# Optimization experiments

Measured on AMD Instinct MI355X. Metric: run time of the kernel, lower is better.

## Reference

```python
import jax, jax.numpy as jnp
import numpy as np

N_NODES = 100000
N_EDGES = 3200000
IN_CH = 256
OUT_CH = 10


def setup_inputs() -> dict:
    key = jax.random.key(0)
    k1, k2, k3, k4 = jax.random.split(key, 4)
    x = jax.random.normal(k1, (N_NODES, IN_CH), dtype=jnp.float32)
    edge_index = jax.random.randint(k2, (2, N_EDGES), 0, N_NODES, dtype=jnp.int64)
    W_mu = jax.random.normal(k3, (IN_CH, OUT_CH), dtype=jnp.float32) * (1.0 / np.sqrt(IN_CH))
    b_mu = jnp.zeros((OUT_CH,), dtype=jnp.float32)
    W_logstd = jax.random.normal(k4, (IN_CH, OUT_CH), dtype=jnp.float32) * (1.0 / np.sqrt(IN_CH))
    b_logstd = jnp.zeros((OUT_CH,), dtype=jnp.float32)
    return {"x": x, "edge_index": edge_index, "W_mu": W_mu, "b_mu": b_mu,
            "W_logstd": W_logstd, "b_logstd": b_logstd}


def _gcn_norm(edge_index, num_nodes):
    # PyG gcn_norm: add self loops, deg from target (col), norm = d^-1/2[row]*d^-1/2[col]
    loop = jnp.arange(num_nodes, dtype=edge_index.dtype)
    row = jnp.concatenate([edge_index[0], loop])  # source nodes
    col = jnp.concatenate([edge_index[1], loop])  # target nodes
    deg = jax.ops.segment_sum(jnp.ones_like(col, dtype=jnp.float32), col,
                              num_segments=num_nodes)
    dinv = jax.lax.rsqrt(jnp.maximum(deg, 1.0))  # self loops guarantee deg>=1
    norm = dinv[row] * dinv[col]  # [E+N]
    return row, col, norm


def _gcn_conv(x, W, b, row, col, norm, num_nodes):
    h = x @ W                               # [N, out]  linear transform first
    msg = h[row] * norm[:, None]            # gather + scale, [E+N, out]
    out = jax.ops.segment_sum(msg, col, num_segments=num_nodes)  # scatter-add
    return out + b


def reference(x, edge_index, W_mu, b_mu, W_logstd, b_logstd):
    n = x.shape[0]
    row, col, norm = _gcn_norm(edge_index, n)
    mu = _gcn_conv(x, W_mu, b_mu, row, col, norm, n)
    logstd = _gcn_conv(x, W_logstd, b_logstd, row, col, norm, n)
    return mu, logstd
```

## Files before the change

kernel.cpp:

```cpp
#include <hip/hip_runtime.h>
#include <math.h>

#define N_NODES 100000
#define N_EDGES 3200000
#define IN_CH 256
#define NC 20
#define OC 10
#define NPB 128
#define NBUCK 782
#define CAP 4864

#define CHUNK3 8192
#define NCHUNK3 391

__global__ __launch_bounds__(256) void k_initptr(int* __restrict__ bptr) {
    int i = blockIdx.x * 256 + threadIdx.x;
    if (i < NBUCK) bptr[i] = i * CAP;
}

__global__ __launch_bounds__(1024) void k_bin3(const int* __restrict__ row,
                                               const int* __restrict__ col,
                                               int* __restrict__ bptr,
                                               int* __restrict__ bpairs) {
    __shared__ int   lh[NBUCK];
    __shared__ int   lscan[NBUCK];
    __shared__ int   gmino[NBUCK];
    __shared__ int   stage[CHUNK3];
    __shared__ unsigned short sbkt[CHUNK3];

    int t = threadIdx.x;
    int e0 = blockIdx.x * CHUNK3;
    int nE = N_EDGES - e0; if (nE > CHUNK3) nE = CHUNK3;
    int n4 = nE >> 2;
    const int4* c4 = (const int4*)(col + e0);
    const int4* r4 = (const int4*)(row + e0);

    for (int i = t; i < NBUCK; i += 1024) lh[i] = 0;
    __syncthreads();

    for (int j = t; j < n4; j += 1024) {
        int4 c = c4[j];
        atomicAdd(&lh[c.x >> 7], 1); atomicAdd(&lh[c.y >> 7], 1);
        atomicAdd(&lh[c.z >> 7], 1); atomicAdd(&lh[c.w >> 7], 1);
    }
    __syncthreads();

    int cnt = 0;
    if (t < NBUCK) { cnt = lh[t]; lscan[t] = cnt; }
    __syncthreads();
    for (int o = 1; o < NBUCK; o <<= 1) {
        int add = 0;
        if (t < NBUCK && t >= o) add = lscan[t - o];
        __syncthreads();
        if (t < NBUCK) lscan[t] += add;
        __syncthreads();
    }
    if (t < NBUCK) {
        int lofs = lscan[t] - cnt;
        int gbase = cnt ? atomicAdd(&bptr[t], cnt) : 0;
        gmino[t] = gbase - lofs;
        lh[t] = lofs;
    }
    __syncthreads();

    for (int j = t; j < n4; j += 1024) {
        int4 c = c4[j];
        int4 r = r4[j];
        int b0 = c.x >> 7, b1 = c.y >> 7, b2 = c.z >> 7, b3 = c.w >> 7;
        int s0 = atomicAdd(&lh[b0], 1);
        int s1 = atomicAdd(&lh[b1], 1);
        int s2 = atomicAdd(&lh[b2], 1);
        int s3 = atomicAdd(&lh[b3], 1);
        stage[s0] = (r.x << 7) | (c.x & 127); sbkt[s0] = (unsigned short)b0;
        stage[s1] = (r.y << 7) | (c.y & 127); sbkt[s1] = (unsigned short)b1;
        stage[s2] = (r.z << 7) | (c.z & 127); sbkt[s2] = (unsigned short)b2;
        stage[s3] = (r.w << 7) | (c.w & 127); sbkt[s3] = (unsigned short)b3;
    }
    __syncthreads();

    for (int j = t; j < nE; j += 1024) {
        int b = sbkt[j];
        int dst = gmino[b] + j;
        if (dst < (b + 1) * CAP) bpairs[dst] = stage[j];
    }
}

__global__ __launch_bounds__(256) void k_deg(const int* __restrict__ bptr,
                                             const int* __restrict__ bpairs,
                                             float* __restrict__ dinv) {
    __shared__ int lc[NPB];
    int b = blockIdx.x, t = threadIdx.x;
    if (t < NPB) lc[t] = 0;
    __syncthreads();
    int start = b * CAP;
    int n = bptr[b] - start; if (n > CAP) n = CAP;
    for (int p = t; p < n; p += 256)
        atomicAdd(&lc[bpairs[start + p] & 127], 1);
    __syncthreads();
    int node = b * NPB + t;
    if (t < NPB && node < N_NODES)
        dinv[node] = rsqrtf((float)(lc[t] + 1));
}

__device__ __forceinline__ unsigned bfpack(float a, float b) {
    unsigned ua = __float_as_uint(a), ub = __float_as_uint(b);
    ua = (ua + 0x7FFFu + ((ua >> 16) & 1u)) >> 16;
    ub = (ub + 0x7FFFu + ((ub >> 16) & 1u)) >> 16;
    return ua | (ub << 16);
}
__device__ __forceinline__ float bflo(unsigned p) { return __uint_as_float(p << 16); }
__device__ __forceinline__ float bfhi(unsigned p) { return __uint_as_float(p & 0xFFFF0000u); }

__global__ __launch_bounds__(256) void k_gemm3(const float* __restrict__ x,
                                               const float* __restrict__ Wmu,
                                               const float* __restrict__ Wls,
                                               const float* __restrict__ dinv,
                                               unsigned* __restrict__ hbf) {
    __shared__ float sW[NC * 272];
    int t = threadIdx.x;
    for (int idx = t; idx < IN_CH * OC; idx += 256) {
        int k = idx / OC, c = idx - k * OC;
        int kk = k >> 6, j = k & 63;
        sW[c * 272 + kk * 68 + j]          = Wmu[idx];
        sW[(c + OC) * 272 + kk * 68 + j]   = Wls[idx];
    }
    __syncthreads();

    int kk = t & 3;
    int slot = t >> 2;
    int n0 = blockIdx.x * 256 + slot;

    int nd[4];
#pragma unroll
    for (int u = 0; u < 4; u++) {
        int n = n0 + u * 64;
        nd[u] = (n < N_NODES) ? n : (N_NODES - 1);
    }

    float acc[4][NC];
#pragma unroll
    for (int u = 0; u < 4; u++)
#pragma unroll
        for (int c = 0; c < NC; c++) acc[u][c] = 0.0f;

    const float4* x4 = (const float4*)x;

#pragma unroll 4
    for (int j4 = 0; j4 < 16; j4++) {
        float4 xv0 = x4[(size_t)nd[0] * 64 + kk * 16 + j4];
        float4 xv1 = x4[(size_t)nd[1] * 64 + kk * 16 + j4];
        float4 xv2 = x4[(size_t)nd[2] * 64 + kk * 16 + j4];
        float4 xv3 = x4[(size_t)nd[3] * 64 + kk * 16 + j4];
#pragma unroll
        for (int c = 0; c < NC; c++) {
            float4 w = *(const float4*)&sW[c * 272 + kk * 68 + j4 * 4];
            acc[0][c] += xv0.x * w.x + xv0.y * w.y + xv0.z * w.z + xv0.w * w.w;
            acc[1][c] += xv1.x * w.x + xv1.y * w.y + xv1.z * w.z + xv1.w * w.w;
            acc[2][c] += xv2.x * w.x + xv2.y * w.y + xv2.z * w.z + xv2.w * w.w;
            acc[3][c] += xv3.x * w.x + xv3.y * w.y + xv3.z * w.z + xv3.w * w.w;
        }
    }

#pragma unroll
    for (int u = 0; u < 4; u++)
#pragma unroll
        for (int c = 0; c < NC; c++) {
            acc[u][c] += __shfl_xor(acc[u][c], 2);
            acc[u][c] += __shfl_xor(acc[u][c], 1);
        }

    if (kk == 0) {
#pragma unroll
        for (int u = 0; u < 4; u++) {
            int n = n0 + u * 64;
            if (n >= N_NODES) continue;
            float d = dinv[n];
            unsigned* hp = hbf + (size_t)n * 10;
            *(uint2*)(hp + 0) = make_uint2(bfpack(acc[u][0] * d,  acc[u][1] * d),
                                           bfpack(acc[u][2] * d,  acc[u][3] * d));
            *(uint2*)(hp + 2) = make_uint2(bfpack(acc[u][4] * d,  acc[u][5] * d),
                                           bfpack(acc[u][6] * d,  acc[u][7] * d));
            *(uint2*)(hp + 4) = make_uint2(bfpack(acc[u][8] * d,  acc[u][9] * d),
                                           bfpack(acc[u][10] * d, acc[u][11] * d));
            *(uint2*)(hp + 6) = make_uint2(bfpack(acc[u][12] * d, acc[u][13] * d),
                                           bfpack(acc[u][14] * d, acc[u][15] * d));
            *(uint2*)(hp + 8) = make_uint2(bfpack(acc[u][16] * d, acc[u][17] * d),
                                           bfpack(acc[u][18] * d, acc[u][19] * d));
        }
    }
}

__global__ __launch_bounds__(256) void k_agg4(const int* __restrict__ bptr,
                                              const int* __restrict__ bpairs,
                                              const unsigned* __restrict__ hbf,
                                              const float* __restrict__ bmu,
                                              const float* __restrict__ bls,
                                              float* __restrict__ out) {
    __shared__ int lcnt[NPB];
    __shared__ int lscan[NPB];
    __shared__ int sCnt[NPB];
    __shared__ int ssrc[CAP];
    int b = blockIdx.x, t = threadIdx.x;
    int start = b * CAP;
    int n = bptr[b] - start; if (n > CAP) n = CAP;

    if (t < NPB) lcnt[t] = 0;
    __syncthreads();
    for (int p = t; p < n; p += 256)
        atomicAdd(&lcnt[bpairs[start + p] & 127], 1);
    __syncthreads();

    int cnt = 0;
    if (t < NPB) { cnt = lcnt[t]; lscan[t] = cnt; sCnt[t] = cnt; }
    __syncthreads();
    for (int o = 1; o < NPB; o <<= 1) {
        int add = 0;
        if (t < NPB && t >= o) add = lscan[t - o];
        __syncthreads();
        if (t < NPB) lscan[t] += add;
        __syncthreads();
    }
    if (t < NPB) lcnt[t] = lscan[t] - cnt;
    __syncthreads();

    for (int p = t; p < n; p += 256) {
        int pk = bpairs[start + p];
        int q = atomicAdd(&lcnt[pk & 127], 1);
        ssrc[q] = ((unsigned)pk) >> 7;
    }
    __syncthreads();

    int nl = t >> 1, half = t & 1;
    int node = b * NPB + nl;
    int ccnt = sCnt[nl];
    int base = lscan[nl] - ccnt;
    int mid = ccnt >> 1;
    int j0 = half ? mid : 0;
    int j1 = half ? ccnt : mid;

    float a[NC];
#pragma unroll
    for (int c = 0; c < NC; c++) a[c] = 0.0f;

#define ADDROW(R)                                                        \
    {                                                                    \
        const unsigned* hp_ = hbf + (size_t)(R) * 10;                    \
        uint2 q0 = *(const uint2*)(hp_ + 0);                             \
        uint2 q1 = *(const uint2*)(hp_ + 2);                             \
        uint2 q2 = *(const uint2*)(hp_ + 4);                             \
        uint2 q3 = *(const uint2*)(hp_ + 6);                             \
        uint2 q4 = *(const uint2*)(hp_ + 8);                             \
        a[0]  += bflo(q0.x); a[1]  += bfhi(q0.x);                        \
        a[2]  += bflo(q0.y); a[3]  += bfhi(q0.y);                        \
        a[4]  += bflo(q1.x); a[5]  += bfhi(q1.x);                        \
        a[6]  += bflo(q1.y); a[7]  += bfhi(q1.y);                        \
        a[8]  += bflo(q2.x); a[9]  += bfhi(q2.x);                        \
        a[10] += bflo(q2.y); a[11] += bfhi(q2.y);                        \
        a[12] += bflo(q3.x); a[13] += bfhi(q3.x);                        \
        a[14] += bflo(q3.y); a[15] += bfhi(q3.y);                        \
        a[16] += bflo(q4.x); a[17] += bfhi(q4.x);                        \
        a[18] += bflo(q4.y); a[19] += bfhi(q4.y);                        \
    }

    int j = j0;
    for (; j + 1 < j1; j += 2) {
        int r0 = ssrc[base + j];
        int r1 = ssrc[base + j + 1];
        ADDROW(r0);
        ADDROW(r1);
    }
    if (j < j1) {
        int r0 = ssrc[base + j];
        ADDROW(r0);
    }
    if (half == 0 && node < N_NODES) ADDROW(node);
#undef ADDROW

#pragma unroll
    for (int c = 0; c < NC; c++) a[c] += __shfl_xor(a[c], 1);

    if (half == 0 && node < N_NODES) {
        float dn = rsqrtf((float)(ccnt + 1));
        float* om = out + (size_t)node * OC;
        float* ol = out + (size_t)N_NODES * OC + (size_t)node * OC;
#pragma unroll
        for (int c = 0; c < OC; c++) {
            om[c] = dn * a[c]      + bmu[c];
            ol[c] = dn * a[c + OC] + bls[c];
        }
    }
}

__global__ __launch_bounds__(256) void k_init_deg(float* __restrict__ deg) {
    int i = blockIdx.x * 256 + threadIdx.x;
    if (i < N_NODES) deg[i] = 1.0f;
}
__global__ __launch_bounds__(256) void k_count(const int* __restrict__ col, float* __restrict__ deg) {
    int e = blockIdx.x * 256 + threadIdx.x;
    if (e < N_EDGES) atomicAdd(&deg[col[e]], 1.0f);
}
__global__ __launch_bounds__(256) void k_dinvk(float* __restrict__ deg) {
    int i = blockIdx.x * 256 + threadIdx.x;
    if (i < N_NODES) deg[i] = rsqrtf(deg[i]);
}
__global__ __launch_bounds__(256) void k_gemm_f32(const float* __restrict__ x,
                                                  const float* __restrict__ Wmu,
                                                  const float* __restrict__ Wls,
                                                  float* __restrict__ h) {
    int node = blockIdx.x * 256 + threadIdx.x;
    if (node >= N_NODES) return;
    const float4* x4 = (const float4*)(x + (size_t)node * IN_CH);
    float acc[NC];
#pragma unroll
    for (int c = 0; c < NC; c++) acc[c] = 0.0f;
    for (int k4 = 0; k4 < IN_CH / 4; k4++) {
        float4 xv = x4[k4];
        float xk[4] = {xv.x, xv.y, xv.z, xv.w};
#pragma unroll
        for (int kk = 0; kk < 4; kk++) {
            const float* wm = Wmu + (k4 * 4 + kk) * OC;
            const float* wl = Wls + (k4 * 4 + kk) * OC;
#pragma unroll
            for (int c = 0; c < OC; c++) {
                acc[c]      += xk[kk] * wm[c];
                acc[c + OC] += xk[kk] * wl[c];
            }
        }
    }
    float* hp = h + (size_t)node * NC;
#pragma unroll
    for (int c = 0; c < NC; c++) hp[c] = acc[c];
}
__global__ __launch_bounds__(256) void k_scatter(const int* __restrict__ row, const int* __restrict__ col,
                                                 const float* __restrict__ dinv, const float* __restrict__ h,
                                                 float* __restrict__ out) {
    int e = blockIdx.x * 256 + threadIdx.x;
    if (e >= N_EDGES) return;
    int r = row[e], c = col[e];
    float s = dinv[r] * dinv[c];
    const float* hp = h + (size_t)r * NC;
    float* om = out + (size_t)c * OC;
    float* ol = om + (size_t)N_NODES * OC;
#pragma unroll
    for (int k = 0; k < OC; k++) atomicAdd(om + k, hp[k] * s);
#pragma unroll
    for (int k = 0; k < OC; k++) atomicAdd(ol + k, hp[OC + k] * s);
}
__global__ __launch_bounds__(256) void k_final(const float* __restrict__ h, const float* __restrict__ dinv,
                                               const float* __restrict__ bmu, const float* __restrict__ bls,
                                               float* __restrict__ out) {
    int i = blockIdx.x * 256 + threadIdx.x;
    if (i >= N_NODES * OC) return;
    int node = i / OC, c = i - node * OC;
    float d = dinv[node];
    float d2 = d * d;
    out[i]                += h[node * NC + c]      * d2 + bmu[c];
    out[N_NODES * OC + i] += h[node * NC + OC + c] * d2 + bls[c];
}

extern "C" void kernel_launch(void* const* d_in, const int* in_sizes, int n_in,
                              void* d_out, int out_size, void* d_ws, size_t ws_size,
                              hipStream_t stream) {
    const float* x   = (const float*)d_in[0];
    const int*   ei  = (const int*)d_in[1];
    const float* Wmu = (const float*)d_in[2];
    const float* bmu = (const float*)d_in[3];
    const float* Wls = (const float*)d_in[4];
    const float* bls = (const float*)d_in[5];
    float* out = (float*)d_out;

    const int* row = ei;
    const int* col = ei + N_EDGES;

    const size_t BPAIRS_OFF = (size_t)(9 << 19);
    const size_t REQ = BPAIRS_OFF + (size_t)NBUCK * CAP * 4;

    if (ws_size >= REQ) {
        char* w = (char*)d_ws;
        int*      bptr   = (int*)(w);
        float*    dinv   = (float*)(w + 8192);
        unsigned* hbf    = (unsigned*)(w + (512 << 10));
        int*      bpairs = (int*)(w + BPAIRS_OFF);

        k_initptr<<<(NBUCK + 255) / 256, 256, 0, stream>>>(bptr);
        k_bin3<<<NCHUNK3, 1024, 0, stream>>>(row, col, bptr, bpairs);
        k_deg<<<NBUCK, 256, 0, stream>>>(bptr, bpairs, dinv);
        k_gemm3<<<(N_NODES + 255) / 256, 256, 0, stream>>>(x, Wmu, Wls, dinv, hbf);
        k_agg4<<<NBUCK, 256, 0, stream>>>(bptr, bpairs, hbf, bmu, bls, out);
    } else {
        float* deg = (float*)d_ws;
        float* h   = (float*)((char*)d_ws + (1 << 20));
        hipMemsetAsync(d_out, 0, (size_t)out_size * sizeof(float), stream);
        k_init_deg<<<(N_NODES + 255) / 256, 256, 0, stream>>>(deg);
        k_count<<<(N_EDGES + 255) / 256, 256, 0, stream>>>(col, deg);
        k_dinvk<<<(N_NODES + 255) / 256, 256, 0, stream>>>(deg);
        k_gemm_f32<<<(N_NODES + 255) / 256, 256, 0, stream>>>(x, Wmu, Wls, h);
        k_scatter<<<(N_EDGES + 255) / 256, 256, 0, stream>>>(row, col, deg, h, out);
        k_final<<<(N_NODES * OC + 255) / 256, 256, 0, stream>>>(h, deg, bmu, bls, out);
    }
}
```

Before: 265.6 us.

## Stage x tiles through shared memory with one node per thread in GEMM

Rewrites the small dense transform so each block loads 256-node by 32-channel tiles of x into padded shared memory with coalesced float4 reads. Each thread then owns one node and accumulates all 20 outputs, reading W as a wave-uniform broadcast from shared memory, which removes the cross-lane shuffle reduction. This trades the old per-thread strided global loads for more barriers and shared-memory traffic.

```diff
diff --git a/kernel.cpp b/kernel.cpp
--- a/kernel.cpp
+++ b/kernel.cpp
@@ -111,82 +111,68 @@
 __device__ __forceinline__ float bflo(unsigned p) { return __uint_as_float(p << 16); }
 __device__ __forceinline__ float bfhi(unsigned p) { return __uint_as_float(p & 0xFFFF0000u); }
 
-__global__ __launch_bounds__(256) void k_gemm3(const float* __restrict__ x,
+__global__ __launch_bounds__(256) void k_gemm5(const float* __restrict__ x,
                                                const float* __restrict__ Wmu,
                                                const float* __restrict__ Wls,
                                                const float* __restrict__ dinv,
                                                unsigned* __restrict__ hbf) {
-    __shared__ float sW[NC * 272];
+    __shared__ float sW[IN_CH * NC];
+    __shared__ float sX[256 * 36];
+
     int t = threadIdx.x;
-    for (int idx = t; idx < IN_CH * OC; idx += 256) {
-        int k = idx / OC, c = idx - k * OC;
-        int kk = k >> 6, j = k & 63;
-        sW[c * 272 + kk * 68 + j]          = Wmu[idx];
-        sW[(c + OC) * 272 + kk * 68 + j]   = Wls[idx];
-    }
-    __syncthreads();
-
-    int kk = t & 3;
-    int slot = t >> 2;
-    int n0 = blockIdx.x * 256 + slot;
-
-    int nd[4];
-#pragma unroll
-    for (int u = 0; u < 4; u++) {
-        int n = n0 + u * 64;
-        nd[u] = (n < N_NODES) ? n : (N_NODES - 1);
-    }
-
-    float acc[4][NC];
-#pragma unroll
-    for (int u = 0; u < 4; u++)
-#pragma unroll
-        for (int c = 0; c < NC; c++) acc[u][c] = 0.0f;
-
-    const float4* x4 = (const float4*)x;
-
-#pragma unroll 4
-    for (int j4 = 0; j4 < 16; j4++) {
-        float4 xv0 = x4[(size_t)nd[0] * 64 + kk * 16 + j4];
-        float4 xv1 = x4[(size_t)nd[1] * 64 + kk * 16 + j4];
-        float4 xv2 = x4[(size_t)nd[2] * 64 + kk * 16 + j4];
-        float4 xv3 = x4[(size_t)nd[3] * 64 + kk * 16 + j4];
-#pragma unroll
-        for (int c = 0; c < NC; c++) {
-            float4 w = *(const float4*)&sW[c * 272 + kk * 68 + j4 * 4];
-            acc[0][c] += xv0.x * w.x + xv0.y * w.y + xv0.z * w.z + xv0.w * w.w;
-            acc[1][c] += xv1.x * w.x + xv1.y * w.y + xv1.z * w.z + xv1.w * w.w;
-            acc[2][c] += xv2.x * w.x + xv2.y * w.y + xv2.z * w.z + xv2.w * w.w;
-            acc[3][c] += xv3.x * w.x + xv3.y * w.y + xv3.z * w.z + xv3.w * w.w;
+    int nbase = blockIdx.x * 256;
+
+    for (int idx = t; idx < IN_CH * NC; idx += 256) {
+        int k = idx / NC, c = idx - (idx / NC) * NC;
+        sW[idx] = (c < OC) ? Wmu[k * OC + c] : Wls[k * OC + (c - OC)];
+    }
+
+    int node = nbase + t;
+
+    float acc[NC];
+#pragma unroll
+    for (int c = 0; c < NC; c++) acc[c] = 0.0f;
+
+    int trow = t >> 3;
+    int tq   = t & 7;
+
+    for (int p = 0; p < 8; p++) {
+        __syncthreads();
+#pragma unroll
+        for (int pass = 0; pass < 8; pass++) {
+            int r = pass * 32 + trow;
+            int gn = nbase + r; if (gn >= N_NODES) gn = N_NODES - 1;
+            float4 v = *(const float4*)(x + (size_t)gn * IN_CH + p * 32 + tq * 4);
+            *(float4*)&sX[r * 36 + tq * 4] = v;
         }
-    }
-
-#pragma unroll
-    for (int u = 0; u < 4; u++)
-#pragma unroll
-        for (int c = 0; c < NC; c++) {
-            acc[u][c] += __shfl_xor(acc[u][c], 2);
-            acc[u][c] += __shfl_xor(acc[u][c], 1);
+        __syncthreads();
+#pragma unroll
+        for (int q = 0; q < 8; q++) {
+            float4 xv = *(const float4*)&sX[t * 36 + q * 4];
+            const float* wq = &sW[(p * 32 + q * 4) * NC];
+            float xj[4] = {xv.x, xv.y, xv.z, xv.w};
+#pragma unroll
+            for (int j = 0; j < 4; j++) {
+#pragma unroll
+                for (int c = 0; c < NC; c++)
+                    acc[c] += xj[j] * wq[j * NC + c];
+            }
         }
-
-    if (kk == 0) {
-#pragma unroll
-        for (int u = 0; u < 4; u++) {
-            int n = n0 + u * 64;
-            if (n >= N_NODES) continue;
-            float d = dinv[n];
-            unsigned* hp = hbf + (size_t)n * 10;
-            *(uint2*)(hp + 0) = make_uint2(bfpack(acc[u][0] * d,  acc[u][1] * d),
-                                           bfpack(acc[u][2] * d,  acc[u][3] * d));
-            *(uint2*)(hp + 2) = make_uint2(bfpack(acc[u][4] * d,  acc[u][5] * d),
-                                           bfpack(acc[u][6] * d,  acc[u][7] * d));
-            *(uint2*)(hp + 4) = make_uint2(bfpack(acc[u][8] * d,  acc[u][9] * d),
-                                           bfpack(acc[u][10] * d, acc[u][11] * d));
-            *(uint2*)(hp + 6) = make_uint2(bfpack(acc[u][12] * d, acc[u][13] * d),
-                                           bfpack(acc[u][14] * d, acc[u][15] * d));
-            *(uint2*)(hp + 8) = make_uint2(bfpack(acc[u][16] * d, acc[u][17] * d),
-                                           bfpack(acc[u][18] * d, acc[u][19] * d));
-        }
+    }
+
+    if (node < N_NODES) {
+        float d = dinv[node];
+        unsigned* hp = hbf + (size_t)node * 10;
+        *(uint2*)(hp + 0) = make_uint2(bfpack(acc[0] * d,  acc[1] * d),
+                                       bfpack(acc[2] * d,  acc[3] * d));
+        *(uint2*)(hp + 2) = make_uint2(bfpack(acc[4] * d,  acc[5] * d),
+                                       bfpack(acc[6] * d,  acc[7] * d));
+        *(uint2*)(hp + 4) = make_uint2(bfpack(acc[8] * d,  acc[9] * d),
+                                       bfpack(acc[10] * d, acc[11] * d));
+        *(uint2*)(hp + 6) = make_uint2(bfpack(acc[12] * d, acc[13] * d),
+                                       bfpack(acc[14] * d, acc[15] * d));
+        *(uint2*)(hp + 8) = make_uint2(bfpack(acc[16] * d, acc[17] * d),
+                                       bfpack(acc[18] * d, acc[19] * d));
     }
 }
 
@@ -385,7 +371,7 @@
         k_initptr<<<(NBUCK + 255) / 256, 256, 0, stream>>>(bptr);
         k_bin3<<<NCHUNK3, 1024, 0, stream>>>(row, col, bptr, bpairs);
         k_deg<<<NBUCK, 256, 0, stream>>>(bptr, bpairs, dinv);
-        k_gemm3<<<(N_NODES + 255) / 256, 256, 0, stream>>>(x, Wmu, Wls, dinv, hbf);
+        k_gemm5<<<(N_NODES + 255) / 256, 256, 0, stream>>>(x, Wmu, Wls, dinv, hbf);
         k_agg4<<<NBUCK, 256, 0, stream>>>(bptr, bpairs, hbf, bmu, bls, out);
     } else {
         float* deg = (float*)d_ws;
```

Measured after the change: 275.7 us. 1.04x slower.
